# Kernel tuning notes

Measured on AMD Instinct MI355X. Metric: run time of the kernel, lower is better.

Reference implementation:

```python
import jax, jax.numpy as jnp
import numpy as np

THRESHOLD = 0.5     # overlap_thresh
NEG_POS = 3         # negative:positive ratio
VAR = (0.1, 0.2)    # cfg['variance']


def point_form(pr):
    # cxcywh -> xmin,ymin,xmax,ymax
    return jnp.concatenate([pr[:, :2] - pr[:, 2:] / 2, pr[:, :2] + pr[:, 2:] / 2], axis=1)


def jaccard(a, b):
    # a: [N,4] point-form truths, b: [P,4] point-form priors -> IoU [N,P]
    lt = jnp.maximum(a[:, None, :2], b[None, :, :2])
    rb = jnp.minimum(a[:, None, 2:], b[None, :, 2:])
    wh = jnp.clip(rb - lt, 0.0)
    inter = wh[..., 0] * wh[..., 1]
    area_a = ((a[:, 2] - a[:, 0]) * (a[:, 3] - a[:, 1]))[:, None]
    area_b = ((b[:, 2] - b[:, 0]) * (b[:, 3] - b[:, 1]))[None, :]
    return inter / (area_a + area_b - inter)


def encode(matched, priors):
    # matched: [P,4] point-form, priors: [P,4] cxcywh
    g_cxcy = ((matched[:, :2] + matched[:, 2:]) / 2 - priors[:, :2]) / (VAR[0] * priors[:, 2:])
    g_wh = jnp.log((matched[:, 2:] - matched[:, :2]) / priors[:, 2:]) / VAR[1]
    return jnp.concatenate([g_cxcy, g_wh], axis=1)


def match_one(truths, labels, priors):
    # truths [N,4], labels [N], priors [P,4] cxcywh
    N = truths.shape[0]
    P = priors.shape[0]
    overlaps = jaccard(truths, point_form(priors))          # [N,P]
    best_prior_idx = jnp.argmax(overlaps, axis=1)           # [N] best prior per truth
    best_truth_overlap = jnp.max(overlaps, axis=0)          # [P]
    best_truth_idx = jnp.argmax(overlaps, axis=0)           # [P]
    # ensure each truth's best prior is kept (overlap forced to 2)
    best_truth_overlap = best_truth_overlap.at[best_prior_idx].set(2.0)
    hit = best_prior_idx[:, None] == jnp.arange(P)[None, :]  # [N,P]
    chosen = jnp.max(jnp.where(hit, jnp.arange(N)[:, None], -1), axis=0)
    best_truth_idx = jnp.where(chosen >= 0, chosen, best_truth_idx)
    matched = truths[best_truth_idx]                        # [P,4]
    conf = labels[best_truth_idx].astype(jnp.int32) + 1
    conf = jnp.where(best_truth_overlap < THRESHOLD, 0, conf)
    return encode(matched, priors), conf


def smooth_l1(x):
    ax = jnp.abs(x)
    return jnp.where(ax < 1.0, 0.5 * ax * ax, ax - 0.5)


def multibox_loss(loc_data, conf_data, priors, targets):
    num, P, C = conf_data.shape
    truths = targets[..., :4]
    labels = targets[..., 4]
    loc_t, conf_t = jax.vmap(match_one, in_axes=(0, 0, None))(truths, labels, priors)
    pos = conf_t > 0                                        # [B,P]

    # localization loss over positives
    loss_l = jnp.sum(jnp.where(pos[..., None], smooth_l1(loc_data - loc_t), 0.0))

    # hard-negative mining score: logsumexp - conf[label clamped to {0,1}]
    batch_conf = jax.lax.stop_gradient(conf_data).reshape(-1, C)
    conf_flat = conf_t.reshape(-1)
    clamped = jnp.where(conf_flat != 0, 1, conf_flat)
    # replicate torch nonzero()-indexing quirk: row 0 also set to 1 if any positive exists
    clamped = clamped.at[0].set(jnp.where(jnp.any(conf_flat != 0), 1, clamped[0]))
    lse = jax.scipy.special.logsumexp(batch_conf, axis=1)
    loss_c = lse - jnp.take_along_axis(batch_conf, clamped[:, None], axis=1)[:, 0]
    loss_c = loss_c.reshape(num, P)
    loss_c = jnp.where(pos, 0.0, loss_c)
    # rank of each prior by descending mining loss
    idx_rank = jnp.argsort(jnp.argsort(-loss_c, axis=1), axis=1)
    num_pos = jnp.sum(pos.astype(jnp.int32), axis=1, keepdims=True)  # [B,1]
    num_neg = jnp.clip(NEG_POS * num_pos, None, P - 1)
    neg = idx_rank < num_neg
    sel = pos | neg

    # confidence cross-entropy over selected priors, original labels as targets
    logp = jax.nn.log_softmax(conf_data, axis=-1)           # [B,P,C]
    ce = -jnp.take_along_axis(logp, conf_t[..., None], axis=-1)[..., 0]
    loss_conf = jnp.sum(jnp.where(sel, ce, 0.0))

    Nf = jnp.sum(num_pos).astype(jnp.float32)
    return loss_l / Nf, loss_conf / Nf


def setup_inputs() -> dict:
    key = jax.random.key(0)
    k1, k2, k3, k4, k5, k6, k7 = jax.random.split(key, 7)
    B, P, C, NOBJ = 128, 8732, 21, 20
    loc_data = jax.random.normal(k1, (B, P, 4), jnp.float32)
    conf_data = jax.random.normal(k2, (B, P, C), jnp.float32)
    pcxy = jax.random.uniform(k3, (P, 2), jnp.float32, 0.05, 0.95)
    pwh = jax.random.uniform(k4, (P, 2), jnp.float32, 0.05, 0.4)
    priors = jnp.concatenate([pcxy, pwh], axis=1)           # cxcywh
    mins = jax.random.uniform(k5, (B, NOBJ, 2), jnp.float32, 0.0, 0.6)
    wh = jax.random.uniform(k6, (B, NOBJ, 2), jnp.float32, 0.05, 0.35)
    lab = jax.random.randint(k7, (B, NOBJ), 0, C - 1).astype(jnp.float32)
    targets = jnp.concatenate([mins, mins + wh, lab[..., None]], axis=-1)
    return {"loc_data": loc_data, "conf_data": conf_data, "priors": priors, "targets": targets}


def reference(loc_data, conf_data, priors, targets):
    return multibox_loss(loc_data, conf_data, priors, targets)
```

## Files before the change

### kernel.cpp

```cpp
#include <hip/hip_runtime.h>

#define PP 8732
#define NB 20
#define NC 21
#define BTH 256
#define NCH 35
#define BTS 1024
#define NWS (BTS/64)


__device__ __forceinline__ float sl1(float d){
  float a = fabsf(d);
  return a < 1.0f ? 0.5f*a*a : a - 0.5f;
}

extern "C" __global__ void __launch_bounds__(BTH)
mb_main(const float* __restrict__ conf_data,
        const float* __restrict__ priors,
        const float* __restrict__ targets,
        float* __restrict__ rankneg,
        unsigned char* __restrict__ meta,
        unsigned long long* __restrict__ keys2)
{
  const int b = blockIdx.x, chunk = blockIdx.y;
  const int tid = threadIdx.x, lane = tid & 63, wid = tid >> 6;
  const int q0 = chunk*BTH + wid*64;
  const int cnt = (q0 < PP) ? ((PP - q0 < 64) ? (PP - q0) : 64) : 0;

  __shared__ float s_buf[4][64*NC];
  __shared__ float4 s_tr4[NB];
  __shared__ unsigned long long s_keys[4][NB];

  if (tid < NB*4){
    int n = tid>>2, k2 = tid&3;
    ((float*)s_tr4)[tid] = targets[((long)b*NB + n)*5 + k2];
  }
  __syncthreads();

  if (cnt == 64){
    const float4* cb4 = reinterpret_cast<const float4*>(conf_data + ((long)b*PP + q0)*NC);
    float4* sb4 = reinterpret_cast<float4*>(s_buf[wid]);
    #pragma unroll
    for (int ii=0; ii<6; ii++){
      int i = ii*64 + lane;
      if (i < 336) sb4[i] = cb4[i];
    }
  } else if (cnt > 0){
    const float4* cb4 = reinterpret_cast<const float4*>(conf_data + ((long)b*PP + q0)*NC);
    float4* sb4 = reinterpret_cast<float4*>(s_buf[wid]);
    const int tot4 = (cnt*NC) >> 2;
    for (int i=lane; i<tot4; i+=64) sb4[i] = cb4[i];
  }

  const bool valid = (lane < cnt);
  const int p  = q0 + lane;
  const int pl = valid ? p : 0;

  const float* v = s_buf[wid] + lane*NC;
  float m = v[0];
  #pragma unroll
  for (int c=1;c<NC;c++) m = fmaxf(m, v[c]);
  float s = 0.f;
  #pragma unroll
  for (int c=0;c<NC;c++) s += __expf(v[c]-m);
  float lse = __logf(s) + m;
  if (valid) rankneg[(long)b*PP + p] = lse - v[0];

  float4 pr = reinterpret_cast<const float4*>(priors)[pl];
  float bx1 = pr.x - pr.z*0.5f, by1 = pr.y - pr.w*0.5f;
  float bx2 = pr.x + pr.z*0.5f, by2 = pr.y + pr.w*0.5f;
  float area_b = (bx2-bx1)*(by2-by1);
  float bestov = -1.0f; int bestn = 0;

  #pragma unroll
  for (int n=0;n<NB;n++){
    float4 t = s_tr4[n];
    float lx=fmaxf(t.x,bx1), ly=fmaxf(t.y,by1);
    float rx=fminf(t.z,bx2), ry=fminf(t.w,by2);
    float iw=fmaxf(rx-lx,0.f), ih=fmaxf(ry-ly,0.f);
    float inter = iw*ih;
    float aa = (t.z-t.x)*(t.w-t.y);
    float uni = aa + area_b - inter;
    float iou = inter * __builtin_amdgcn_rcpf(uni);
    if (iou > bestov){ bestov=iou; bestn=n; }

    float wm = valid ? iou : -1.0f;
    #pragma unroll
    for (int o=32;o;o>>=1) wm = fmaxf(wm, __shfl_xor(wm, o, 64));
    unsigned long long mk = __ballot(valid && (iou == wm));
    if (mk){
      if (lane == __ffsll((long long)mk)-1)
        s_keys[wid][n] = ((unsigned long long)__float_as_uint(iou)<<32)
                       | (unsigned long long)(0xFFFFFFFFu - (unsigned)p);
    } else if (lane==0){
      s_keys[wid][n] = 0ULL;
    }
  }

  if (valid) meta[(long)b*PP + p] = (unsigned char)((bestn<<1) | (bestov >= 0.5f ? 1 : 0));

  __syncthreads();
  if (tid < NB){
    unsigned long long mx = s_keys[0][tid];
    #pragma unroll
    for (int w=1;w<4;w++) if (s_keys[w][tid] > mx) mx = s_keys[w][tid];
    keys2[((long)b*NCH + chunk)*NB + tid] = mx;
  }
}

extern "C" __global__ void __launch_bounds__(BTS)
mb_select(const float* __restrict__ loc_data,
          const float* __restrict__ conf_data,
          const float* __restrict__ priors,
          const float* __restrict__ targets,
          const float* __restrict__ rankneg,
          const unsigned char* __restrict__ meta,
          const unsigned long long* __restrict__ keys2,
          float* __restrict__ rowres, int* __restrict__ ticket,
          float* __restrict__ out, int Bn)
{
  const int b = blockIdx.x, tid = threadIdx.x, lane = tid & 63, wid = tid >> 6;
  __shared__ float s_val[PP];
  __shared__ unsigned int s_meta4[PP/4];
  __shared__ float4 s_tr4[NB];
  __shared__ float s_lab[NB];
  __shared__ int   s_bp[NB];
  __shared__ int   s_cnt[2][NWS];
  __shared__ float s_fa[NWS], s_fb[NWS], s_fc[NWS];
  __shared__ int   s_ia[NWS];
  __shared__ float s_rowll, s_rowpc, s_delta;
  __shared__ int   s_npos, s_spec, s_last;
  unsigned char* s_meta = (unsigned char*)s_meta4;
  float4* sv4 = reinterpret_cast<float4*>(s_val);

  const float4* rr = reinterpret_cast<const float4*>(rankneg + (long)b*PP);
  for (int i=tid;i<PP/4;i+=BTS) sv4[i]=rr[i];
  const unsigned int* mr = reinterpret_cast<const unsigned int*>(meta + (long)b*PP);
  for (int i=tid;i<PP/4;i+=BTS) s_meta4[i]=mr[i];
  if (tid < NB*5){
    int n = tid/5, k2 = tid-n*5;
    float vv = targets[((long)b*NB+n)*5+k2];
    if (k2<4) ((float*)&s_tr4[n])[k2]=vv; else s_lab[n]=vv;
  }
  if (tid < NB){
    unsigned long long mx = 0ULL;
    #pragma unroll
    for (int c=0;c<NCH;c++){
      unsigned long long kk = keys2[((long)b*NCH + c)*NB + tid];
      if (kk > mx) mx = kk;
    }
    s_bp[tid] = (int)(0xFFFFFFFFu - (unsigned)(mx & 0xFFFFFFFFULL));
  }
  if (tid==0){ s_spec=0; s_delta=0.f; }
  __syncthreads();

  if (tid==0){
    for (int n=0;n<NB;n++) s_meta[s_bp[n]] = (unsigned char)((n<<1)|1);
  }
  __syncthreads();

  float ll=0.f, pc=0.f; int np=0;
  for (int p=tid;p<PP;p+=BTS){
    int mt = s_meta[p];
    if (mt & 1){
      np++;
      int n = mt>>1;
      int ct = (int)s_lab[n] + 1;
      const float* cp = conf_data + ((long)b*PP+p)*NC;
      float v0 = cp[0], vct = cp[ct];
      pc += s_val[p] + v0 - vct;
      float4 t = s_tr4[n];
      float4 pr = reinterpret_cast<const float4*>(priors)[p];
      float4 ld = reinterpret_cast<const float4*>(loc_data)[(long)b*PP+p];
      float g0 = ((t.x+t.z)*0.5f - pr.x)/(0.1f*pr.z);
      float g1 = ((t.y+t.w)*0.5f - pr.y)/(0.1f*pr.w);
      float g2 = __logf((t.z-t.x)/pr.z)/0.2f;
      float g3 = __logf((t.w-t.y)/pr.w)/0.2f;
      ll += sl1(ld.x-g0)+sl1(ld.y-g1)+sl1(ld.z-g2)+sl1(ld.w-g3);
      s_val[p] = 0.f;
    } else if (b==0 && p==0){
      float v0 = conf_data[0], v1 = conf_data[1];
      float r0 = s_val[0];
      float r0p = r0 + v0 - v1;
      s_delta = r0 - r0p;
      s_spec = 1;
      s_val[0] = r0p;
    }
  }
  #pragma unroll
  for (int o=32;o;o>>=1){
    ll += __shfl_down(ll,o,64);
    pc += __shfl_down(pc,o,64);
    np += __shfl_down(np,o,64);
  }
  if (lane==0){ s_fa[wid]=ll; s_fb[wid]=pc; s_ia[wid]=np; }
  __syncthreads();
  if (tid==0){
    float a=0.f,c2=0.f; int ni=0;
    for (int w=0;w<NWS;w++){ a+=s_fa[w]; c2+=s_fb[w]; ni+=s_ia[w]; }
    s_rowll=a; s_rowpc=c2; s_npos=ni;
  }
  __syncthreads();
  const int num_pos = s_npos;
  int k = num_pos*3; if (k > PP-1) k = PP-1;

  float negsum = 0.f;
  if (k > 0){
    unsigned lo=0u, hi=0x7f800000u;
    int it=0;
    while (lo < hi){
      unsigned mid = lo + ((hi - lo + 1u) >> 1);
      int c=0;
      for (int i=tid;i<PP/4;i+=BTS){
        float4 x = sv4[i];
        c += (__float_as_uint(x.x)>=mid) + (__float_as_uint(x.y)>=mid)
           + (__float_as_uint(x.z)>=mid) + (__float_as_uint(x.w)>=mid);
      }
      #pragma unroll
      for (int o=32;o;o>>=1) c += __shfl_down(c,o,64);
      int sl2 = it&1;
      if (lane==0) s_cnt[sl2][wid]=c;
      __syncthreads();
      int tot=0;
      #pragma unroll
      for (int w=0;w<NWS;w++) tot += s_cnt[sl2][w];
      if (tot >= k) lo = mid; else hi = mid - 1u;
      it++;
    }
    const unsigned vstar = lo;

    int cg=0; float sg=0.f;
    for (int i=tid;i<PP/4;i+=BTS){
      float4 x = sv4[i];
      if (__float_as_uint(x.x)>vstar){cg++;sg+=x.x;}
      if (__float_as_uint(x.y)>vstar){cg++;sg+=x.y;}
      if (__float_as_uint(x.z)>vstar){cg++;sg+=x.z;}
      if (__float_as_uint(x.w)>vstar){cg++;sg+=x.w;}
    }
    #pragma unroll
    for (int o=32;o;o>>=1){ cg += __shfl_down(cg,o,64); sg += __shfl_down(sg,o,64); }
    __syncthreads();
    if (lane==0){ s_ia[wid]=cg; s_fa[wid]=sg; }
    __syncthreads();
    if (tid==0){
      int cG=0; float sumG=0.f;
      for (int w=0;w<NWS;w++){ cG+=s_ia[w]; sumG+=s_fa[w]; }
      int tie = k - cG;
      negsum = sumG + (float)tie * __uint_as_float(vstar);
      if (b==0 && s_spec && __float_as_uint(s_val[0]) >= vstar) negsum += s_delta;
    }
  }

  if (tid==0){
    rowres[b*4+0] = s_rowll;
    rowres[b*4+1] = s_rowpc + negsum;
    rowres[b*4+2] = (float)num_pos;
    __threadfence();
    int t = atomicAdd(ticket, 1);
    s_last = (t == gridDim.x - 1) ? 1 : 0;
  }
  __syncthreads();

  if (s_last){
    __threadfence();
    float a0=0.f, a1=0.f, a2=0.f;
    for (int i=tid;i<Bn;i+=BTS){
      a0 += rowres[i*4+0]; a1 += rowres[i*4+1]; a2 += rowres[i*4+2];
    }
    #pragma unroll
    for (int o=32;o;o>>=1){
      a0 += __shfl_down(a0,o,64);
      a1 += __shfl_down(a1,o,64);
      a2 += __shfl_down(a2,o,64);
    }
    if (lane==0){ s_fa[wid]=a0; s_fb[wid]=a1; s_fc[wid]=a2; }
    __syncthreads();
    if (tid==0){
      float A0=0.f,A1=0.f,A2=0.f;
      for (int w=0;w<NWS;w++){ A0+=s_fa[w]; A1+=s_fb[w]; A2+=s_fc[w]; }
      out[0] = A0/A2;
      out[1] = A1/A2;
    }
  }
}

extern "C" void kernel_launch(void* const* d_in, const int* in_sizes, int n_in,
                              void* d_out, int out_size, void* d_ws, size_t ws_size,
                              hipStream_t stream) {
  const float* loc     = (const float*)d_in[0];
  const float* conf    = (const float*)d_in[1];
  const float* priors  = (const float*)d_in[2];
  const float* targets = (const float*)d_in[3];
  float* out = (float*)d_out;
  int B = in_sizes[0] / (PP*4);

  char* ws = (char*)d_ws;
  int*   ticket = (int*)ws;
  float* rowres = (float*)(ws + 64);
  unsigned long long* keys2 = (unsigned long long*)(ws + 4096);
  size_t off_rank = 4096 + (size_t)B*NCH*NB*8;
  float* rankneg = (float*)(ws + off_rank);
  unsigned char* metaa = (unsigned char*)(ws + off_rank + (size_t)B*PP*4);

  hipMemsetAsync(d_ws, 0, 64, stream);
  hipLaunchKernelGGL(mb_main,   dim3(B, NCH), dim3(BTH), 0, stream,
                     conf, priors, targets, rankneg, metaa, keys2);
  hipLaunchKernelGGL(mb_select, dim3(B), dim3(BTS), 0, stream,
                     loc, conf, priors, targets, rankneg, metaa, keys2,
                     rowres, ticket, out, B);
}
```

Measured before the change: 218.9 us.

## Use DPP wave max, cache rank values in registers for radix search

In mb_main, the shuffle-based wave max reduction becomes a DPP row/bcast sequence with readlane, key slots are zero-initialized up front instead of per iteration, and the loop over boxes is no longer force-unrolled. In mb_select, each thread loads its three float4 rank values from shared memory into registers once, before the binary search. Every search iteration then counts from registers instead of rereading LDS. This trades extra register pressure and code complexity for fewer shuffles and LDS reads. The removed unroll may cost some ILP.

```diff
diff --git a/kernel.cpp b/kernel.cpp
--- a/kernel.cpp
+++ b/kernel.cpp
@@ -8,10 +8,20 @@
 #define BTS 1024
 #define NWS (BTS/64)
 
-
 __device__ __forceinline__ float sl1(float d){
   float a = fabsf(d);
   return a < 1.0f ? 0.5f*a*a : a - 0.5f;
+}
+
+__device__ __forceinline__ float wave_max64(float x){
+  int t;
+  t = __builtin_amdgcn_update_dpp(0, __float_as_int(x), 0x111, 0xF, 0xF, true); x = fmaxf(x, __int_as_float(t));
+  t = __builtin_amdgcn_update_dpp(0, __float_as_int(x), 0x112, 0xF, 0xF, true); x = fmaxf(x, __int_as_float(t));
+  t = __builtin_amdgcn_update_dpp(0, __float_as_int(x), 0x114, 0xF, 0xF, true); x = fmaxf(x, __int_as_float(t));
+  t = __builtin_amdgcn_update_dpp(0, __float_as_int(x), 0x118, 0xF, 0xF, true); x = fmaxf(x, __int_as_float(t));
+  t = __builtin_amdgcn_update_dpp(0, __float_as_int(x), 0x142, 0xF, 0xF, true); x = fmaxf(x, __int_as_float(t));
+  t = __builtin_amdgcn_update_dpp(0, __float_as_int(x), 0x143, 0xF, 0xF, true); x = fmaxf(x, __int_as_float(t));
+  return __int_as_float(__builtin_amdgcn_readlane(__float_as_int(x), 63));
 }
 
 extern "C" __global__ void __launch_bounds__(BTH)
@@ -35,6 +45,7 @@
     int n = tid>>2, k2 = tid&3;
     ((float*)s_tr4)[tid] = targets[((long)b*NB + n)*5 + k2];
   }
+  if (lane < NB) s_keys[wid][lane] = 0ULL;
   __syncthreads();
 
   if (cnt == 64){
@@ -72,7 +83,6 @@
   float area_b = (bx2-bx1)*(by2-by1);
   float bestov = -1.0f; int bestn = 0;
 
-  #pragma unroll
   for (int n=0;n<NB;n++){
     float4 t = s_tr4[n];
     float lx=fmaxf(t.x,bx1), ly=fmaxf(t.y,by1);
@@ -80,20 +90,17 @@
     float iw=fmaxf(rx-lx,0.f), ih=fmaxf(ry-ly,0.f);
     float inter = iw*ih;
     float aa = (t.z-t.x)*(t.w-t.y);
-    float uni = aa + area_b - inter;
-    float iou = inter * __builtin_amdgcn_rcpf(uni);
+    float iou = inter * __builtin_amdgcn_rcpf(aa + area_b - inter);
     if (iou > bestov){ bestov=iou; bestn=n; }
 
-    float wm = valid ? iou : -1.0f;
-    #pragma unroll
-    for (int o=32;o;o>>=1) wm = fmaxf(wm, __shfl_xor(wm, o, 64));
-    unsigned long long mk = __ballot(valid && (iou == wm));
+    float iouv = valid ? iou : -1.0f;
+    float wmax = wave_max64(iouv);
+    unsigned long long mk = __ballot(valid && (iou == wmax));
     if (mk){
-      if (lane == __ffsll((long long)mk)-1)
+      int wlane = __ffsll((long long)mk) - 1;
+      if (lane == wlane)
         s_keys[wid][n] = ((unsigned long long)__float_as_uint(iou)<<32)
                        | (unsigned long long)(0xFFFFFFFFu - (unsigned)p);
-    } else if (lane==0){
-      s_keys[wid][n] = 0ULL;
     }
   }
 
@@ -195,6 +202,12 @@
   }
   if (lane==0){ s_fa[wid]=ll; s_fb[wid]=pc; s_ia[wid]=np; }
   __syncthreads();
+
+  float4 rv0 = sv4[tid];
+  float4 rv1 = sv4[tid+1024];
+  float4 rv2 = (tid < PP/4-2048) ? sv4[tid+2048]
+                                 : make_float4(0.f,0.f,0.f,0.f);
+
   if (tid==0){
     float a=0.f,c2=0.f; int ni=0;
     for (int w=0;w<NWS;w++){ a+=s_fa[w]; c2+=s_fb[w]; ni+=s_ia[w]; }
@@ -210,12 +223,12 @@
     int it=0;
     while (lo < hi){
       unsigned mid = lo + ((hi - lo + 1u) >> 1);
-      int c=0;
-      for (int i=tid;i<PP/4;i+=BTS){
-        float4 x = sv4[i];
-        c += (__float_as_uint(x.x)>=mid) + (__float_as_uint(x.y)>=mid)
-           + (__float_as_uint(x.z)>=mid) + (__float_as_uint(x.w)>=mid);
-      }
+      int c = (__float_as_uint(rv0.x)>=mid) + (__float_as_uint(rv0.y)>=mid)
+            + (__float_as_uint(rv0.z)>=mid) + (__float_as_uint(rv0.w)>=mid)
+            + (__float_as_uint(rv1.x)>=mid) + (__float_as_uint(rv1.y)>=mid)
+            + (__float_as_uint(rv1.z)>=mid) + (__float_as_uint(rv1.w)>=mid)
+            + (__float_as_uint(rv2.x)>=mid) + (__float_as_uint(rv2.y)>=mid)
+            + (__float_as_uint(rv2.z)>=mid) + (__float_as_uint(rv2.w)>=mid);
       #pragma unroll
       for (int o=32;o;o>>=1) c += __shfl_down(c,o,64);
       int sl2 = it&1;
@@ -230,13 +243,11 @@
     const unsigned vstar = lo;
 
     int cg=0; float sg=0.f;
-    for (int i=tid;i<PP/4;i+=BTS){
-      float4 x = sv4[i];
-      if (__float_as_uint(x.x)>vstar){cg++;sg+=x.x;}
-      if (__float_as_uint(x.y)>vstar){cg++;sg+=x.y;}
-      if (__float_as_uint(x.z)>vstar){cg++;sg+=x.z;}
-      if (__float_as_uint(x.w)>vstar){cg++;sg+=x.w;}
-    }
+    #define ACC(x) if (__float_as_uint(x)>vstar){cg++;sg+=(x);}
+    ACC(rv0.x) ACC(rv0.y) ACC(rv0.z) ACC(rv0.w)
+    ACC(rv1.x) ACC(rv1.y) ACC(rv1.z) ACC(rv1.w)
+    ACC(rv2.x) ACC(rv2.y) ACC(rv2.z) ACC(rv2.w)
+    #undef ACC
     #pragma unroll
     for (int o=32;o;o>>=1){ cg += __shfl_down(cg,o,64); sg += __shfl_down(sg,o,64); }
     __syncthreads();
```

Result: faster. 214.2 us (-2.2%).
